# Kernel optimization log

Hardware: AMD Instinct MI355X
Metric: run time of the kernel (lower is better)

The kernel has to match this reference:

```python
import jax, jax.numpy as jnp
import numpy as np

N_NODES = 100000
N_EDGES = 1600000
N_GRAPHS = 64
IN_CH, HID_CH, OUT_CH, N_CLS = 128, 128, 64, 2


def setup_inputs() -> dict:
    key = jax.random.key(0)
    ks = jax.random.split(key, 8)
    x = jax.random.normal(ks[0], (N_NODES, IN_CH), dtype=jnp.float32)
    edge_index = jax.random.randint(ks[1], (2, N_EDGES), 0, N_NODES)
    batch = jnp.sort(jax.random.randint(ks[2], (N_NODES,), 0, N_GRAPHS))
    glorot = lambda k, shp: jax.random.normal(k, shp, dtype=jnp.float32) / np.float32(np.sqrt(shp[0]))
    return {
        "x": x, "edge_index": edge_index, "batch": batch,
        "W1": glorot(ks[3], (IN_CH, HID_CH)), "b1": jnp.zeros((HID_CH,), jnp.float32),
        "W2": glorot(ks[4], (HID_CH, HID_CH)), "b2": jnp.zeros((HID_CH,), jnp.float32),
        "W3": glorot(ks[5], (HID_CH, OUT_CH)), "b3": jnp.zeros((OUT_CH,), jnp.float32),
        "Wfc": glorot(ks[6], (OUT_CH, N_CLS)), "bfc": jnp.zeros((N_CLS,), jnp.float32),
    }


def gcn_conv(x, src, dst, W, b):
    """PyG GCNConv: add self-loops, D^{-1/2} (A+I) D^{-1/2} (x W) + b."""
    n = x.shape[0]
    h = x @ W  # [N, out]
    # degree with self-loops: 1 + in-degree at dst
    deg = jnp.ones((n,), h.dtype).at[dst].add(1.0)
    dinv = jax.lax.rsqrt(deg)  # deg >= 1 always (self-loop)
    norm = dinv[src] * dinv[dst]  # [E]
    agg = jnp.zeros_like(h).at[dst].add(h[src] * norm[:, None])
    agg = agg + h * (dinv * dinv)[:, None]  # self-loop messages
    return agg + b


def global_mean_pool(x, batch, num_graphs):
    s = jax.ops.segment_sum(x, batch, num_segments=num_graphs)
    cnt = jax.ops.segment_sum(jnp.ones((x.shape[0],), x.dtype), batch, num_segments=num_graphs)
    return s / jnp.maximum(cnt, 1.0)[:, None]


def reference(x, edge_index, batch, W1, b1, W2, b2, W3, b3, Wfc, bfc):
    src, dst = edge_index[0], edge_index[1]
    h = jax.nn.relu(gcn_conv(x, src, dst, W1, b1))   # dropout p=0.0 (eval) -> identity
    h = jax.nn.relu(gcn_conv(h, src, dst, W2, b2))
    h = gcn_conv(h, src, dst, W3, b3)
    g = global_mean_pool(h, batch, N_GRAPHS)          # [G, OUT_CH]
    return g @ Wfc + bfc                              # [G, N_CLS]
```

## Files before the change

### kernel.cpp

```cpp
#include <hip/hip_runtime.h>
#include <hip/hip_bf16.h>


#define THREADS 256
#define BSHIFT 9
#define BSIZE 512

typedef __attribute__((ext_vector_type(8))) short short8;
typedef __attribute__((ext_vector_type(16))) float floatx16;

__device__ __forceinline__ unsigned f2bf(float f) {
    unsigned u = __float_as_uint(f);
    return (u + 0x7fffu + ((u >> 16) & 1u)) >> 16;
}

__device__ __forceinline__ void bf8_acc(uint4 v, float* ac) {
    ac[0] += __uint_as_float(v.x << 16);
    ac[1] += __uint_as_float(v.x & 0xffff0000u);
    ac[2] += __uint_as_float(v.y << 16);
    ac[3] += __uint_as_float(v.y & 0xffff0000u);
    ac[4] += __uint_as_float(v.z << 16);
    ac[5] += __uint_as_float(v.z & 0xffff0000u);
    ac[6] += __uint_as_float(v.w << 16);
    ac[7] += __uint_as_float(v.w & 0xffff0000u);
}


__global__ __launch_bounds__(THREADS) void bucket_count(const int* __restrict__ dst,
                                                        int* __restrict__ btotal,
                                                        int E, int nbuck) {
    __shared__ int cnt[BSIZE];
    for (int i = threadIdx.x; i < nbuck; i += THREADS) cnt[i] = 0;
    __syncthreads();
    for (int e = blockIdx.x * THREADS + threadIdx.x; e < E; e += gridDim.x * THREADS)
        atomicAdd(&cnt[dst[e] >> BSHIFT], 1);
    __syncthreads();
    for (int i = threadIdx.x; i < nbuck; i += THREADS) {
        int c = cnt[i];
        if (c) atomicAdd(&btotal[i], c);
    }
}

__global__ __launch_bounds__(512) void bucket_scan(const int* __restrict__ btotal,
                                                   int* __restrict__ bbase,
                                                   int* __restrict__ bcursor,
                                                   int nbuck, int E) {
    __shared__ int lds[512];
    int t = threadIdx.x;
    int v = (t < nbuck) ? btotal[t] : 0;
    lds[t] = v;
    __syncthreads();
    for (int off = 1; off < 512; off <<= 1) {
        int tv = (t >= off) ? lds[t - off] : 0;
        __syncthreads();
        lds[t] += tv;
        __syncthreads();
    }
    if (t < nbuck) {
        int excl = lds[t] - v;
        bbase[t] = excl;
        bcursor[t] = excl;
    }
    if (t == 0) bbase[nbuck] = E;
}

__global__ __launch_bounds__(THREADS) void bucket_scatter(const int* __restrict__ src,
                                                          const int* __restrict__ dst,
                                                          int* __restrict__ bcursor,
                                                          int2* __restrict__ pairs, int E) {
    __shared__ int cnt[BSIZE];
    __shared__ int base[BSIZE];
    for (int i = threadIdx.x; i < BSIZE; i += THREADS) cnt[i] = 0;
    __syncthreads();
    int e0 = blockIdx.x * 2048;
    int myb[8], myrank[8], mysrc[8], mydst[8];
#pragma unroll
    for (int j = 0; j < 8; ++j) {
        int e = e0 + j * THREADS + threadIdx.x;
        myb[j] = -1;
        if (e < E) {
            int d = dst[e];
            mysrc[j] = src[e];
            mydst[j] = d;
            myb[j] = d >> BSHIFT;
            myrank[j] = atomicAdd(&cnt[myb[j]], 1);
        }
    }
    __syncthreads();
    for (int i = threadIdx.x; i < BSIZE; i += THREADS) {
        int c = cnt[i];
        base[i] = c ? atomicAdd(&bcursor[i], c) : 0;
    }
    __syncthreads();
#pragma unroll
    for (int j = 0; j < 8; ++j)
        if (myb[j] >= 0) pairs[(size_t)base[myb[j]] + myrank[j]] = make_int2(mysrc[j], mydst[j]);
}

__global__ __launch_bounds__(512) void bucket_fill(const int2* __restrict__ pairs,
                                                   const int* __restrict__ bbase,
                                                   int* __restrict__ row_start,
                                                   float* __restrict__ dinv,
                                                   int* __restrict__ esrc,
                                                   int N, int E, int nbuck) {
    __shared__ int cnt[BSIZE];
    __shared__ int scn[BSIZE];
    int b = blockIdx.x, t = threadIdx.x;
    int s = bbase[b], e = bbase[b + 1];
    cnt[t] = 0;
    __syncthreads();
    for (int i = s + t; i < e; i += 512) atomicAdd(&cnt[pairs[i].y & (BSIZE - 1)], 1);
    __syncthreads();
    int v = cnt[t];
    scn[t] = v;
    __syncthreads();
    for (int off = 1; off < 512; off <<= 1) {
        int tv = (t >= off) ? scn[t - off] : 0;
        __syncthreads();
        scn[t] += tv;
        __syncthreads();
    }
    int excl = scn[t] - v;
    int g = (b << BSHIFT) + t;
    if (g < N) {
        row_start[g] = s + excl;
        dinv[g] = rsqrtf(1.0f + (float)v);
    }
    if (b == nbuck - 1 && t == 0) row_start[N] = E;
    scn[t] = excl;
    __syncthreads();
    for (int i = s + t; i < e; i += 512) {
        int2 p = pairs[i];
        int r = atomicAdd(&scn[p.y & (BSIZE - 1)], 1);
        esrc[s + r] = p.x;
    }
}

__device__ __forceinline__ void wt_pack(const float* W, uint4* Wtp, int C, int li) {
    int c = li >> 4, ch = li & 15;
    unsigned r[8];
#pragma unroll
    for (int j = 0; j < 8; ++j) r[j] = f2bf(W[(size_t)(ch * 8 + j) * C + c]);
    uint4 o;
    o.x = r[0] | (r[1] << 16);
    o.y = r[2] | (r[3] << 16);
    o.z = r[4] | (r[5] << 16);
    o.w = r[6] | (r[7] << 16);
    Wtp[li] = o;
}

__global__ __launch_bounds__(THREADS) void prep_wt_all(const float* __restrict__ W1,
                                                       const float* __restrict__ W2,
                                                       const float* __restrict__ W3,
                                                       uint4* __restrict__ Wt1,
                                                       uint4* __restrict__ Wt2,
                                                       uint4* __restrict__ Wt3) {
    int idx = blockIdx.x * THREADS + threadIdx.x;
    if (idx < 2048) wt_pack(W1, Wt1, 128, idx);
    else if (idx < 4096) wt_pack(W2, Wt2, 128, idx - 2048);
    else if (idx < 5120) wt_pack(W3, Wt3, 64, idx - 4096);
}

__global__ __launch_bounds__(THREADS) void prep_x(const float* __restrict__ x,
                                                  const float* __restrict__ dinv,
                                                  uint4* __restrict__ Z, int n) {
    int idx = blockIdx.x * THREADS + threadIdx.x;
    if (idx >= n * 16) return;
    int r = idx >> 4, c = idx & 15;
    float dv = dinv[r];
    const float* p = x + (size_t)r * 128 + c * 8;
    float4 a = *(const float4*)p;
    float4 b = *(const float4*)(p + 4);
    uint4 o;
    o.x = f2bf(a.x * dv) | (f2bf(a.y * dv) << 16);
    o.y = f2bf(a.z * dv) | (f2bf(a.w * dv) << 16);
    o.z = f2bf(b.x * dv) | (f2bf(b.y * dv) << 16);
    o.w = f2bf(b.z * dv) | (f2bf(b.w * dv) << 16);
    Z[idx] = o;
}

__global__ __launch_bounds__(THREADS) void fused_layer(const uint4* __restrict__ Z,
                                                       const uint4* __restrict__ Wt,
                                                       const int* __restrict__ row_start,
                                                       const int* __restrict__ esrc,
                                                       const float* __restrict__ dinv,
                                                       const float* __restrict__ bias,
                                                       uint4* __restrict__ out, int n) {
    __shared__ __align__(16) uint4 ldsX[64 * 16];
    int row0 = blockIdx.x * 64;
    int maxr = n - row0;
    if (maxr > 64) maxr = 64;
    int tid = threadIdx.x;
    int lane = tid & 15, grp = tid >> 4;

    for (int round = 0; round < 4; ++round) {
        int r = round * 16 + grp;
        int node = row0 + r;
        int nd = (node < n) ? node : (n - 1);
        float ac[8] = {0, 0, 0, 0, 0, 0, 0, 0};
        bf8_acc(Z[(size_t)nd * 16 + lane], ac);
        int s = row_start[nd], e = row_start[nd + 1];
        int i = s;
        for (; i + 8 <= e; i += 8) {
            int s0 = esrc[i], s1 = esrc[i + 1], s2 = esrc[i + 2], s3 = esrc[i + 3];
            int s4 = esrc[i + 4], s5 = esrc[i + 5], s6 = esrc[i + 6], s7 = esrc[i + 7];
            uint4 v0 = Z[(size_t)s0 * 16 + lane];
            uint4 v1 = Z[(size_t)s1 * 16 + lane];
            uint4 v2 = Z[(size_t)s2 * 16 + lane];
            uint4 v3 = Z[(size_t)s3 * 16 + lane];
            uint4 v4 = Z[(size_t)s4 * 16 + lane];
            uint4 v5 = Z[(size_t)s5 * 16 + lane];
            uint4 v6 = Z[(size_t)s6 * 16 + lane];
            uint4 v7 = Z[(size_t)s7 * 16 + lane];
            bf8_acc(v0, ac); bf8_acc(v1, ac); bf8_acc(v2, ac); bf8_acc(v3, ac);
            bf8_acc(v4, ac); bf8_acc(v5, ac); bf8_acc(v6, ac); bf8_acc(v7, ac);
        }
        for (; i + 4 <= e; i += 4) {
            int s0 = esrc[i], s1 = esrc[i + 1], s2 = esrc[i + 2], s3 = esrc[i + 3];
            uint4 v0 = Z[(size_t)s0 * 16 + lane];
            uint4 v1 = Z[(size_t)s1 * 16 + lane];
            uint4 v2 = Z[(size_t)s2 * 16 + lane];
            uint4 v3 = Z[(size_t)s3 * 16 + lane];
            bf8_acc(v0, ac); bf8_acc(v1, ac); bf8_acc(v2, ac); bf8_acc(v3, ac);
        }
        for (; i < e; ++i) bf8_acc(Z[(size_t)esrc[i] * 16 + lane], ac);
        float dv = dinv[nd];
        uint4 o;
        o.x = f2bf(ac[0] * dv) | (f2bf(ac[1] * dv) << 16);
        o.y = f2bf(ac[2] * dv) | (f2bf(ac[3] * dv) << 16);
        o.z = f2bf(ac[4] * dv) | (f2bf(ac[5] * dv) << 16);
        o.w = f2bf(ac[6] * dv) | (f2bf(ac[7] * dv) << 16);
        ldsX[r * 16 + (lane ^ (r & 7))] = o;
    }
    __syncthreads();

    int l = tid & 63, wv = tid >> 6;
    int l31 = l & 31, half = l >> 5;
    int nt = wv & 1, mt0 = (wv >> 1) * 2;
    floatx16 acc[2];
#pragma unroll
    for (int t = 0; t < 2; ++t)
#pragma unroll
        for (int q = 0; q < 16; ++q) acc[t][q] = 0.0f;
    int xrow = nt * 32 + l31, xsw = xrow & 7;
#pragma unroll
    for (int kt = 0; kt < 8; ++kt) {
        int chunk = kt * 2 + half;
        short8 xf = *(const short8*)&ldsX[xrow * 16 + (chunk ^ xsw)];
#pragma unroll
        for (int t = 0; t < 2; ++t) {
            int c = (mt0 + t) * 32 + l31;
            short8 wf = *(const short8*)&Wt[c * 16 + chunk];
            acc[t] = __builtin_amdgcn_mfma_f32_32x32x16_bf16(wf, xf, acc[t], 0, 0, 0);
        }
    }
    __syncthreads();

    int node = nt * 32 + l31;
    float dv = (node < maxr) ? dinv[row0 + node] : 0.0f;
    char* outb = (char*)ldsX;
#pragma unroll
    for (int t = 0; t < 2; ++t) {
        int cb = (mt0 + t) * 32;
#pragma unroll
        for (int q = 0; q < 4; ++q) {
            float v[4];
#pragma unroll
            for (int m = 0; m < 4; ++m) {
                int ch = cb + 8 * q + 4 * half + m;
                float x_ = acc[t][q * 4 + m] + bias[ch];
                x_ = fmaxf(x_, 0.0f);
                v[m] = x_ * dv;
            }
            uint2 pk = make_uint2(f2bf(v[0]) | (f2bf(v[1]) << 16),
                                  f2bf(v[2]) | (f2bf(v[3]) << 16));
            int chunk = (cb >> 3) + q;
            *(uint2*)(outb + node * 256 + ((chunk ^ (node & 7)) * 16) + half * 8) = pk;
        }
    }
    __syncthreads();
    for (int idx = tid; idx < maxr * 16; idx += THREADS) {
        int r = idx >> 4, c = idx & 15;
        out[(size_t)(row0 + r) * 16 + c] = *(uint4*)(outb + r * 256 + ((c ^ (r & 7)) * 16));
    }
}

__global__ __launch_bounds__(THREADS) void gemm3(const uint4* __restrict__ Z,
                                                 const uint4* __restrict__ Wt,
                                                 uint4* __restrict__ out, int n) {
    __shared__ __align__(16) uint4 ldsX[64 * 16];
    int row0 = blockIdx.x * 64;
    int maxr = n - row0;
    if (maxr > 64) maxr = 64;
    int tid = threadIdx.x;
    for (int idx = tid; idx < 1024; idx += THREADS) {
        int r = idx >> 4, c = idx & 15;
        uint4 o = (r < maxr) ? Z[(size_t)(row0 + r) * 16 + c] : make_uint4(0, 0, 0, 0);
        ldsX[r * 16 + (c ^ (r & 7))] = o;
    }
    __syncthreads();
    int l = tid & 63, wv = tid >> 6;
    int l31 = l & 31, half = l >> 5;
    int nt = wv & 1, mt = wv >> 1;
    floatx16 acc;
#pragma unroll
    for (int q = 0; q < 16; ++q) acc[q] = 0.0f;
    int xrow = nt * 32 + l31, xsw = xrow & 7;
#pragma unroll
    for (int kt = 0; kt < 8; ++kt) {
        int chunk = kt * 2 + half;
        short8 xf = *(const short8*)&ldsX[xrow * 16 + (chunk ^ xsw)];
        int c = mt * 32 + l31;
        short8 wf = *(const short8*)&Wt[c * 16 + chunk];
        acc = __builtin_amdgcn_mfma_f32_32x32x16_bf16(wf, xf, acc, 0, 0, 0);
    }
    __syncthreads();
    int node = nt * 32 + l31;
    char* outb = (char*)ldsX;
    int cb = mt * 32;
#pragma unroll
    for (int q = 0; q < 4; ++q) {
        uint2 pk = make_uint2(f2bf(acc[q * 4 + 0]) | (f2bf(acc[q * 4 + 1]) << 16),
                              f2bf(acc[q * 4 + 2]) | (f2bf(acc[q * 4 + 3]) << 16));
        int chunk = (cb >> 3) + q;
        *(uint2*)(outb + node * 128 + ((chunk ^ (node & 7)) * 16) + half * 8) = pk;
    }
    __syncthreads();
    for (int idx = tid; idx < maxr * 8; idx += THREADS) {
        int r = idx >> 3, c = idx & 7;
        out[(size_t)(row0 + r) * 8 + c] = *(uint4*)(outb + r * 128 + ((c ^ (r & 7)) * 16));
    }
}

__global__ __launch_bounds__(THREADS) void agg_pool(const uint4* __restrict__ Ps,
                                                    const int* __restrict__ row_start,
                                                    const int* __restrict__ esrc,
                                                    const float* __restrict__ dinv,
                                                    const float* __restrict__ bias,
                                                    const int* __restrict__ batch,
                                                    float* __restrict__ gsum, int n) {
    __shared__ float gpart[32][65];
    __shared__ int used[32];
    int tid = threadIdx.x;
    int lane = tid & 7, grp = tid >> 3;
    int node = blockIdx.x * 32 + grp;
    if (tid < 32) used[tid] = 0;
    for (int idx = tid; idx < 2048; idx += THREADS) gpart[idx >> 6][idx & 63] = 0.0f;
    __syncthreads();
    int gmin = batch[blockIdx.x * 32];
    if (node < n) {
        float ac[8] = {0, 0, 0, 0, 0, 0, 0, 0};
        bf8_acc(Ps[(size_t)node * 8 + lane], ac);
        int s = row_start[node], e = row_start[node + 1];
        int i = s;
        for (; i + 8 <= e; i += 8) {
            int s0 = esrc[i], s1 = esrc[i + 1], s2 = esrc[i + 2], s3 = esrc[i + 3];
            int s4 = esrc[i + 4], s5 = esrc[i + 5], s6 = esrc[i + 6], s7 = esrc[i + 7];
            uint4 v0 = Ps[(size_t)s0 * 8 + lane];
            uint4 v1 = Ps[(size_t)s1 * 8 + lane];
            uint4 v2 = Ps[(size_t)s2 * 8 + lane];
            uint4 v3 = Ps[(size_t)s3 * 8 + lane];
            uint4 v4 = Ps[(size_t)s4 * 8 + lane];
            uint4 v5 = Ps[(size_t)s5 * 8 + lane];
            uint4 v6 = Ps[(size_t)s6 * 8 + lane];
            uint4 v7 = Ps[(size_t)s7 * 8 + lane];
            bf8_acc(v0, ac); bf8_acc(v1, ac); bf8_acc(v2, ac); bf8_acc(v3, ac);
            bf8_acc(v4, ac); bf8_acc(v5, ac); bf8_acc(v6, ac); bf8_acc(v7, ac);
        }
        for (; i + 4 <= e; i += 4) {
            int s0 = esrc[i], s1 = esrc[i + 1], s2 = esrc[i + 2], s3 = esrc[i + 3];
            uint4 v0 = Ps[(size_t)s0 * 8 + lane];
            uint4 v1 = Ps[(size_t)s1 * 8 + lane];
            uint4 v2 = Ps[(size_t)s2 * 8 + lane];
            uint4 v3 = Ps[(size_t)s3 * 8 + lane];
            bf8_acc(v0, ac); bf8_acc(v1, ac); bf8_acc(v2, ac); bf8_acc(v3, ac);
        }
        for (; i < e; ++i) bf8_acc(Ps[(size_t)esrc[i] * 8 + lane], ac);
        float dv = dinv[node];
        float4 b0 = ((const float4*)bias)[lane * 2];
        float4 b1 = ((const float4*)bias)[lane * 2 + 1];
        float h[8];
        h[0] = fmaf(dv, ac[0], b0.x); h[1] = fmaf(dv, ac[1], b0.y);
        h[2] = fmaf(dv, ac[2], b0.z); h[3] = fmaf(dv, ac[3], b0.w);
        h[4] = fmaf(dv, ac[4], b1.x); h[5] = fmaf(dv, ac[5], b1.y);
        h[6] = fmaf(dv, ac[6], b1.z); h[7] = fmaf(dv, ac[7], b1.w);
        int g = batch[node];
        int slot = g - gmin;
        if (slot < 32) {
            if (lane == 0) used[slot] = 1;
#pragma unroll
            for (int j = 0; j < 8; ++j) atomicAdd(&gpart[slot][lane * 8 + j], h[j]);
        } else {
#pragma unroll
            for (int j = 0; j < 8; ++j) atomicAdd(&gsum[(size_t)g * 64 + lane * 8 + j], h[j]);
        }
    }
    __syncthreads();
    for (int idx = tid; idx < 2048; idx += THREADS) {
        int s = idx >> 6, ch = idx & 63;
        if (used[s]) atomicAdd(&gsum[(size_t)(gmin + s) * 64 + ch], gpart[s][ch]);
    }
}

__device__ __forceinline__ int dev_lower_bound(const int* a, int n, int key) {
    int lo = 0, hi = n;
    while (lo < hi) {
        int mid = (lo + hi) >> 1;
        if (a[mid] < key) lo = mid + 1;
        else hi = mid;
    }
    return lo;
}

__global__ __launch_bounds__(128) void finalize_fc(const float* __restrict__ gsum,
                                                   const int* __restrict__ batch, int n,
                                                   const float* __restrict__ Wfc,
                                                   const float* __restrict__ bfc,
                                                   float* __restrict__ out) {
    __shared__ float gm[64 * 64];
    __shared__ float cnt[64];
    int t = threadIdx.x;
    if (t < 64)
        cnt[t] = (float)(dev_lower_bound(batch, n, t + 1) - dev_lower_bound(batch, n, t));
    __syncthreads();
    for (int i = t; i < 64 * 64; i += 128) gm[i] = gsum[i] / fmaxf(cnt[i >> 6], 1.0f);
    __syncthreads();
    int g = t >> 1, cls = t & 1;
    float acc = bfc[cls];
    for (int c = 0; c < 64; ++c) acc = fmaf(gm[g * 64 + c], Wfc[c * 2 + cls], acc);
    out[g * 2 + cls] = acc;
}

extern "C" void kernel_launch(void* const* d_in, const int* in_sizes, int n_in,
                              void* d_out, int out_size, void* d_ws, size_t ws_size,
                              hipStream_t stream) {
    const float* x    = (const float*)d_in[0];
    const int*   ei   = (const int*)d_in[1];
    const int*   batch= (const int*)d_in[2];
    const float* W1   = (const float*)d_in[3];
    const float* b1   = (const float*)d_in[4];
    const float* W2   = (const float*)d_in[5];
    const float* b2   = (const float*)d_in[6];
    const float* W3   = (const float*)d_in[7];
    const float* b3   = (const float*)d_in[8];
    const float* Wfc  = (const float*)d_in[9];
    const float* bfc  = (const float*)d_in[10];
    float* out = (float*)d_out;

    const int N = in_sizes[2];
    const int E = in_sizes[1] / 2;
    const int* esrc_in = ei;
    const int* edst_in = ei + E;
    const int nbuck = (N + BSIZE - 1) >> BSHIFT;

    uint4* bufA      = (uint4*)d_ws;
    uint4* bufB      = bufA + (size_t)N * 16;
    uint4* bufC      = bufB + (size_t)N * 16;
    int2*  pairs     = (int2*)(bufC + (size_t)N * 8);
    int*   esrc      = (int*)(pairs + E);
    int*   row_start = esrc + E;
    float* dinv      = (float*)(row_start + N + 1);
    int*   btotal    = (int*)(dinv + N);
    int*   bbase     = btotal + 512;
    int*   bcursor   = bbase + 513;
    float* gsum      = (float*)(bcursor + 512);
    uint4* Wt1       = (uint4*)(gsum + 64 * 64 + 2);
    uint4* Wt2       = Wt1 + 2048;
    uint4* Wt3       = Wt2 + 2048;

    hipMemsetAsync(btotal, 0, 512 * sizeof(int), stream);
    hipMemsetAsync(gsum, 0, 64 * 64 * sizeof(float), stream);
    bucket_count<<<512, THREADS, 0, stream>>>(edst_in, btotal, E, nbuck);
    bucket_scan<<<1, 512, 0, stream>>>(btotal, bbase, bcursor, nbuck, E);
    bucket_scatter<<<(E + 2047) / 2048, THREADS, 0, stream>>>(esrc_in, edst_in, bcursor, pairs, E);
    bucket_fill<<<nbuck, 512, 0, stream>>>(pairs, bbase, row_start, dinv, esrc, N, E, nbuck);
    prep_wt_all<<<20, THREADS, 0, stream>>>(W1, W2, W3, Wt1, Wt2, Wt3);
    prep_x<<<(N * 16 + THREADS - 1) / THREADS, THREADS, 0, stream>>>(x, dinv, bufA, N);

    const int GB = (N + 63) / 64;

    fused_layer<<<GB, THREADS, 0, stream>>>(bufA, Wt1, row_start, esrc, dinv, b1, bufB, N);
    fused_layer<<<GB, THREADS, 0, stream>>>(bufB, Wt2, row_start, esrc, dinv, b2, bufA, N);
    gemm3<<<GB, THREADS, 0, stream>>>(bufA, Wt3, bufC, N);
    agg_pool<<<(N + 31) / 32, THREADS, 0, stream>>>(bufC, row_start, esrc, dinv, b3, batch, gsum, N);

    finalize_fc<<<1, 128, 0, stream>>>(gsum, batch, N, Wfc, bfc, out);
}
```

Measured before the change: 440.7 us.

## Group nodes by in-degree via counting-sort permutation for balanced aggregation

Adds a degree histogram, scan and scatter that build a permutation of nodes sorted by in-degree. The two fused aggregation+GEMM layers then process rows in that order, so each 64-row block and each 16-lane group walks edge lists of similar length, which reduces wave divergence and tail imbalance. Output rows are written back to their original node positions through the permutation. The cost is three extra small kernels, an indirect index load, and less locality in the output writes and neighbour reads.

```diff
diff --git a/kernel.cpp b/kernel.cpp
--- a/kernel.cpp
+++ b/kernel.cpp
@@ -133,6 +133,48 @@
         int2 p = pairs[i];
         int r = atomicAdd(&scn[p.y & (BSIZE - 1)], 1);
         esrc[s + r] = p.x;
+    }
+}
+
+__global__ __launch_bounds__(THREADS) void deg_hist(const int* __restrict__ row_start,
+                                                    int* __restrict__ hist, int N) {
+    __shared__ int h[256];
+    h[threadIdx.x] = 0;
+    __syncthreads();
+    int i = blockIdx.x * THREADS + threadIdx.x;
+    if (i < N) {
+        int d = min(row_start[i + 1] - row_start[i], 255);
+        atomicAdd(&h[d], 1);
+    }
+    __syncthreads();
+    int c = h[threadIdx.x];
+    if (c) atomicAdd(&hist[threadIdx.x], c);
+}
+
+__global__ __launch_bounds__(256) void deg_scan(const int* __restrict__ hist,
+                                                int* __restrict__ dcur) {
+    __shared__ int lds[256];
+    int t = threadIdx.x;
+    int v = hist[t];
+    lds[t] = v;
+    __syncthreads();
+    for (int off = 1; off < 256; off <<= 1) {
+        int tv = (t >= off) ? lds[t - off] : 0;
+        __syncthreads();
+        lds[t] += tv;
+        __syncthreads();
+    }
+    dcur[t] = lds[t] - v;
+}
+
+__global__ __launch_bounds__(THREADS) void perm_scatter(const int* __restrict__ row_start,
+                                                        int* __restrict__ dcur,
+                                                        int* __restrict__ perm, int N) {
+    int i = blockIdx.x * THREADS + threadIdx.x;
+    if (i < N) {
+        int d = min(row_start[i + 1] - row_start[i], 255);
+        int pos = atomicAdd(&dcur[d], 1);
+        perm[pos] = i;
     }
 }
 
@@ -185,18 +227,19 @@
                                                        const int* __restrict__ esrc,
                                                        const float* __restrict__ dinv,
                                                        const float* __restrict__ bias,
+                                                       const int* __restrict__ perm,
                                                        uint4* __restrict__ out, int n) {
     __shared__ __align__(16) uint4 ldsX[64 * 16];
+    __shared__ int nodes_s[64];
     int row0 = blockIdx.x * 64;
-    int maxr = n - row0;
-    if (maxr > 64) maxr = 64;
     int tid = threadIdx.x;
     int lane = tid & 15, grp = tid >> 4;
 
     for (int round = 0; round < 4; ++round) {
         int r = round * 16 + grp;
-        int node = row0 + r;
-        int nd = (node < n) ? node : (n - 1);
+        int gi = row0 + r;
+        int nd = perm[(gi < n) ? gi : (n - 1)];
+        if (lane == 0) nodes_s[r] = nd;
         float ac[8] = {0, 0, 0, 0, 0, 0, 0, 0};
         bf8_acc(Z[(size_t)nd * 16 + lane], ac);
         int s = row_start[nd], e = row_start[nd + 1];
@@ -256,8 +299,8 @@
     }
     __syncthreads();
 
-    int node = nt * 32 + l31;
-    float dv = (node < maxr) ? dinv[row0 + node] : 0.0f;
+    int lrow = nt * 32 + l31;
+    float dv = (row0 + lrow < n) ? dinv[nodes_s[lrow]] : 0.0f;
     char* outb = (char*)ldsX;
 #pragma unroll
     for (int t = 0; t < 2; ++t) {
@@ -275,13 +318,15 @@
             uint2 pk = make_uint2(f2bf(v[0]) | (f2bf(v[1]) << 16),
                                   f2bf(v[2]) | (f2bf(v[3]) << 16));
             int chunk = (cb >> 3) + q;
-            *(uint2*)(outb + node * 256 + ((chunk ^ (node & 7)) * 16) + half * 8) = pk;
-        }
-    }
-    __syncthreads();
+            *(uint2*)(outb + lrow * 256 + ((chunk ^ (lrow & 7)) * 16) + half * 8) = pk;
+        }
+    }
+    __syncthreads();
+    int maxr = n - row0;
+    if (maxr > 64) maxr = 64;
     for (int idx = tid; idx < maxr * 16; idx += THREADS) {
         int r = idx >> 4, c = idx & 15;
-        out[(size_t)(row0 + r) * 16 + c] = *(uint4*)(outb + r * 256 + ((c ^ (r & 7)) * 16));
+        out[(size_t)nodes_s[r] * 16 + c] = *(uint4*)(outb + r * 256 + ((c ^ (r & 7)) * 16));
     }
 }
 
@@ -460,27 +505,34 @@
     int*   esrc      = (int*)(pairs + E);
     int*   row_start = esrc + E;
     float* dinv      = (float*)(row_start + N + 1);
-    int*   btotal    = (int*)(dinv + N);
+    int*   perm      = (int*)(dinv + N);
+    int*   btotal    = perm + N;
     int*   bbase     = btotal + 512;
     int*   bcursor   = bbase + 513;
-    float* gsum      = (float*)(bcursor + 512);
-    uint4* Wt1       = (uint4*)(gsum + 64 * 64 + 2);
+    int*   dhist     = bcursor + 512;
+    int*   dcur      = dhist + 256;
+    float* gsum      = (float*)(dcur + 256);
+    uint4* Wt1       = (uint4*)(gsum + 64 * 64);
     uint4* Wt2       = Wt1 + 2048;
     uint4* Wt3       = Wt2 + 2048;
 
     hipMemsetAsync(btotal, 0, 512 * sizeof(int), stream);
+    hipMemsetAsync(dhist, 0, 256 * sizeof(int), stream);
     hipMemsetAsync(gsum, 0, 64 * 64 * sizeof(float), stream);
     bucket_count<<<512, THREADS, 0, stream>>>(edst_in, btotal, E, nbuck);
     bucket_scan<<<1, 512, 0, stream>>>(btotal, bbase, bcursor, nbuck, E);
     bucket_scatter<<<(E + 2047) / 2048, THREADS, 0, stream>>>(esrc_in, edst_in, bcursor, pairs, E);
     bucket_fill<<<nbuck, 512, 0, stream>>>(pairs, bbase, row_start, dinv, esrc, N, E, nbuck);
+    deg_hist<<<(N + THREADS - 1) / THREADS, THREADS, 0, stream>>>(row_start, dhist, N);
+    deg_scan<<<1, 256, 0, stream>>>(dhist, dcur);
+    perm_scatter<<<(N + THREADS - 1) / THREADS, THREADS, 0, stream>>>(row_start, dcur, perm, N);
     prep_wt_all<<<20, THREADS, 0, stream>>>(W1, W2, W3, Wt1, Wt2, Wt3);
     prep_x<<<(N * 16 + THREADS - 1) / THREADS, THREADS, 0, stream>>>(x, dinv, bufA, N);
 
     const int GB = (N + 63) / 64;
 
-    fused_layer<<<GB, THREADS, 0, stream>>>(bufA, Wt1, row_start, esrc, dinv, b1, bufB, N);
-    fused_layer<<<GB, THREADS, 0, stream>>>(bufB, Wt2, row_start, esrc, dinv, b2, bufA, N);
+    fused_layer<<<GB, THREADS, 0, stream>>>(bufA, Wt1, row_start, esrc, dinv, b1, perm, bufB, N);
+    fused_layer<<<GB, THREADS, 0, stream>>>(bufB, Wt2, row_start, esrc, dinv, b2, perm, bufA, N);
     gemm3<<<GB, THREADS, 0, stream>>>(bufA, Wt3, bufC, N);
     agg_pool<<<(N + 31) / 32, THREADS, 0, stream>>>(bufC, row_start, esrc, dinv, b3, batch, gsum, N);
 
```

After: 731.8 us. 1.66x slower.
